# Performance work log

Hardware: AMD Instinct MI355X
Metric: run time of the kernel (lower is better)

The kernel has to match this reference:

```python
import jax, jax.numpy as jnp
import numpy as np

KEY_DIM = 64
SCALE_PER_SEQ = 1.0 / np.sqrt(KEY_DIM).astype(np.float32)
SCALE_OVER_SEQS = 1.0 / np.sqrt(KEY_DIM).astype(np.float32)


def setup_inputs() -> dict:
    key = jax.random.key(0)
    ks = jax.random.split(key, 6)
    b, i, t, j, d, dv, kd = 4, 512, 32, 256, 512, 512, KEY_DIM
    w_scale = 0.05
    return {
        "input_seq": jax.random.normal(ks[0], (b, i, d), jnp.float32),
        "memory_x": jax.random.normal(ks[1], (b, t, j, d), jnp.float32),
        "memory_y": jax.random.normal(ks[2], (b, t, j, dv), jnp.float32),
        "Wq": jax.random.normal(ks[3], (d, kd), jnp.float32) * w_scale,
        "bq": jnp.zeros((kd,), jnp.float32),
        "Wk": jax.random.normal(ks[4], (d, kd), jnp.float32) * w_scale,
        "bk": jnp.zeros((kd,), jnp.float32),
        "Wv": jax.random.normal(ks[5], (dv, dv), jnp.float32) * w_scale,
        "bv": jnp.zeros((dv,), jnp.float32),
    }


def reference(input_seq, memory_x, memory_y, Wq, bq, Wk, bk, Wv, bv):
    # Projections (Dense layers)
    queries = input_seq @ Wq + bq          # [b, i, kd]
    keys = memory_x @ Wk + bk              # [b, t, j, kd]
    values = memory_y @ Wv + bv            # [b, t, j, dv]

    # Level 1: within-sequence attention
    attn_mat = jnp.einsum('bik,btjk->btij', queries, keys)          # [b, t, i, j]
    per_seq_attn = jax.nn.softmax(SCALE_PER_SEQ * attn_mat, axis=-1)
    per_seq_retrieved = jnp.einsum('btij,btjk->btik', per_seq_attn, values)  # [b, t, i, dv]

    # Level 2: over-sequences attention (max-reduce over j, softmax over t)
    mem_seq_attn = jnp.max(attn_mat, axis=-1)                       # [b, t, i]
    mem_seq_attn = jax.nn.softmax(SCALE_OVER_SEQS * mem_seq_attn, axis=1)

    retrieved = jnp.einsum('bti,btik->bik', mem_seq_attn, per_seq_retrieved)  # [b, i, dv]
    return retrieved
```

## Files before the change

### kernel.cpp

```cpp
#include <hip/hip_runtime.h>
#include <cstdint>

#define B_ 4
#define I_ 512
#define T_ 32
#define J_ 256
#define D_ 512
#define DV_ 512
#define KD_ 64
#define TJ_ (T_*J_)
#define BI_ (B_*I_)
#define MK_ (B_*T_*J_)

typedef unsigned short u16;
typedef __attribute__((ext_vector_type(8))) u16 u16x8;
typedef __attribute__((ext_vector_type(4))) u16 u16x4;
typedef __attribute__((ext_vector_type(8))) short bf16x8;
typedef __attribute__((ext_vector_type(4))) float f32x4;

__device__ __forceinline__ u16 f2bf(float f){
  unsigned u = __float_as_uint(f);
  u += 0x7fffu + ((u >> 16) & 1u);
  return (u16)(u >> 16);
}
__device__ __forceinline__ float bf2f(u16 h){ return __uint_as_float(((unsigned)h) << 16); }

#define GLD16(gsrc, ldst) __builtin_amdgcn_global_load_lds( \
    (const __attribute__((address_space(1))) unsigned int*)(gsrc), \
    (__attribute__((address_space(3))) unsigned int*)(ldst), 16, 0, 0)

__global__ __launch_bounds__(256) void k_prep(const float* __restrict__ Y, u16* __restrict__ Yt,
                                              const float* __restrict__ Wq, const float* __restrict__ Wk,
                                              const float* __restrict__ Wv, u16* __restrict__ wqt,
                                              u16* __restrict__ wkt, u16* __restrict__ wvt){
  __shared__ __align__(16) u16 tileT[64][72];
  int bid = blockIdx.x;
  int tid = threadIdx.x;
  if (bid < 4096){
    int kx = bid & 127, ny = (bid >> 7) & 7, b = bid >> 10;
    int k0 = kx*64, n0 = ny*64;
    #pragma unroll
    for (int s=0;s<4;++s){
      int idx = tid + s*256; int r = idx>>4, c4 = idx&15;
      const float4 v = *(const float4*)&Y[((size_t)b*TJ_ + k0 + r)*DV_ + n0 + c4*4];
      tileT[c4*4+0][r] = f2bf(v.x);
      tileT[c4*4+1][r] = f2bf(v.y);
      tileT[c4*4+2][r] = f2bf(v.z);
      tileT[c4*4+3][r] = f2bf(v.w);
    }
    __syncthreads();
    #pragma unroll
    for (int s=0;s<2;++s){
      int idx = tid + s*256; int rn = idx>>3, c8 = idx&7;
      *(u16x8*)&Yt[((size_t)b*DV_ + n0 + rn)*TJ_ + k0 + c8*8] = *(const u16x8*)&tileT[rn][c8*8];
    }
  } else {
    int gid = (bid - 4096)*256 + tid;
    if (gid < 32768){
      int n = gid >> 9, k = gid & 511;
      wqt[gid] = f2bf(Wq[(size_t)k*64 + n]);
    } else if (gid < 65536){
      int g = gid - 32768;
      int n = g >> 9, k = g & 511;
      wkt[g] = f2bf(Wk[(size_t)k*64 + n]);
    } else {
      int g = gid - 65536;
      int n = g >> 9, k = g & 511;
      wvt[g] = f2bf(Wv[(size_t)k*512 + n]);
    }
  }
}

__global__ __launch_bounds__(256) void k_proj(const float* __restrict__ mx, const float* __restrict__ iseq,
                                              const u16* __restrict__ wkt, const u16* __restrict__ wqt,
                                              const float* __restrict__ bk, const float* __restrict__ bq,
                                              u16* __restrict__ kbf, u16* __restrict__ qbf){
  __shared__ __align__(16) u16 As[32][72];
  __shared__ __align__(16) u16 Bs[64][72];
  int bid = blockIdx.x;
  const float* A; const u16* Bt; const float* bias; u16* C; int row0;
  if (bid < 1024){ A = mx;   Bt = wkt; bias = bk; C = kbf; row0 = bid*32; }
  else           { A = iseq; Bt = wqt; bias = bq; C = qbf; row0 = (bid-1024)*32; }
  int tid = threadIdx.x;
  int lane = tid & 63, wv = tid >> 6;
  int lrow = lane & 15, lk8 = (lane >> 4) * 8;
  int mf = wv >> 1, nfb = (wv & 1) * 2;
  int ar = tid >> 4, ac4 = tid & 15;
  int br = tid >> 3, bc8 = tid & 7;
  f32x4 acc[2];
  acc[0] = (f32x4){0.f,0.f,0.f,0.f}; acc[1] = (f32x4){0.f,0.f,0.f,0.f};

  float4 fa[2][2]; u16x8 fb[2][2];
  #define PROJ_LOAD(pp, k0) { \
    fa[pp][0] = *(const float4*)&A[(size_t)(row0 + ar)*512 + (k0) + ac4*4]; \
    fa[pp][1] = *(const float4*)&A[(size_t)(row0 + ar + 16)*512 + (k0) + ac4*4]; \
    fb[pp][0] = *(const u16x8*)&Bt[(size_t)br*512 + (k0) + bc8*8]; \
    fb[pp][1] = *(const u16x8*)&Bt[(size_t)(br+32)*512 + (k0) + bc8*8]; }

  PROJ_LOAD(0, 0)
  #pragma unroll
  for (int t=0;t<8;++t){
    const int p = t & 1;
    if (t) __syncthreads();
    if (t < 7) PROJ_LOAD(p^1, (t+1)*64)
    #pragma unroll
    for (int s=0;s<2;++s){
      u16x4 o; o[0]=f2bf(fa[p][s].x); o[1]=f2bf(fa[p][s].y); o[2]=f2bf(fa[p][s].z); o[3]=f2bf(fa[p][s].w);
      *(u16x4*)&As[ar + 16*s][ac4*4] = o;
      *(u16x8*)&Bs[br + 32*s][bc8*8] = fb[p][s];
    }
    __syncthreads();
    #pragma unroll
    for (int kk=0;kk<2;++kk){
      bf16x8 a = *(const bf16x8*)&As[mf*16 + lrow][kk*32 + lk8];
      #pragma unroll
      for (int n2=0;n2<2;++n2){
        bf16x8 bb = *(const bf16x8*)&Bs[(nfb+n2)*16 + lrow][kk*32 + lk8];
        acc[n2] = __builtin_amdgcn_mfma_f32_16x16x32_bf16(a, bb, acc[n2], 0, 0, 0);
      }
    }
  }
  #undef PROJ_LOAD
  #pragma unroll
  for (int n2=0;n2<2;++n2)
    #pragma unroll
    for (int r=0;r<4;++r){
      int row = row0 + mf*16 + (lane>>4)*4 + r;
      int col = (nfb+n2)*16 + lrow;
      C[(size_t)row*64 + col] = f2bf(acc[n2][r] + bias[col]);
    }
}

__global__ __launch_bounds__(256) void k_score(const u16* __restrict__ Qbf, const u16* __restrict__ Kbf,
                                               u16* __restrict__ P, float* __restrict__ mb, float* __restrict__ zb){
  __shared__ __align__(16) u16 Qs[64][72];
  __shared__ __align__(16) u16 Ks[256][72];
  __shared__ float smax[4][64];
  __shared__ float ssum[4][64];
  __shared__ float mrow[64];
  int tid = threadIdx.x;
  int i0 = blockIdx.x*64, t = blockIdx.y, b = blockIdx.z;
  int lane = tid & 63, wv = tid >> 6;
  int lrow = lane & 15, lk = (lane >> 4) * 8;

  #pragma unroll
  for (int s=0;s<2;++s){
    int idx = tid + s*256; int r = idx>>3, c8 = idx&7;
    *(u16x8*)&Qs[r][c8*8] = *(const u16x8*)&Qbf[((size_t)b*I_ + i0 + r)*KD_ + c8*8];
  }
  #pragma unroll
  for (int s=0;s<8;++s){
    int idx = tid + s*256; int r = idx>>3, c8 = idx&7;
    *(u16x8*)&Ks[r][c8*8] = *(const u16x8*)&Kbf[(((size_t)b*T_ + t)*J_ + r)*KD_ + c8*8];
  }
  __syncthreads();

  f32x4 acc[4][4];
  #pragma unroll
  for (int i=0;i<4;++i)
    #pragma unroll
    for (int j=0;j<4;++j) acc[i][j] = (f32x4){0.f,0.f,0.f,0.f};

  #pragma unroll
  for (int kk=0;kk<2;++kk){
    bf16x8 a[4], bb[4];
    #pragma unroll
    for (int mf=0;mf<4;++mf) a[mf] = *(const bf16x8*)&Qs[mf*16 + lrow][kk*32 + lk];
    #pragma unroll
    for (int nf=0;nf<4;++nf) bb[nf] = *(const bf16x8*)&Ks[wv*64 + nf*16 + lrow][kk*32 + lk];
    #pragma unroll
    for (int mf=0;mf<4;++mf)
      #pragma unroll
      for (int nf=0;nf<4;++nf)
        acc[mf][nf] = __builtin_amdgcn_mfma_f32_16x16x32_bf16(a[mf], bb[nf], acc[mf][nf], 0, 0, 0);
  }

  #pragma unroll
  for (int mf=0;mf<4;++mf)
    #pragma unroll
    for (int r=0;r<4;++r){
      float v = acc[mf][0][r];
      #pragma unroll
      for (int nf=1;nf<4;++nf) v = fmaxf(v, acc[mf][nf][r]);
      v = fmaxf(v, __shfl_xor(v, 1));
      v = fmaxf(v, __shfl_xor(v, 2));
      v = fmaxf(v, __shfl_xor(v, 4));
      v = fmaxf(v, __shfl_xor(v, 8));
      if (lrow == 0) smax[wv][mf*16 + (lane>>4)*4 + r] = v;
    }
  __syncthreads();
  if (tid < 64){
    float m = fmaxf(fmaxf(smax[0][tid], smax[1][tid]), fmaxf(smax[2][tid], smax[3][tid]));
    mrow[tid] = m;
    mb[((size_t)b*T_ + t)*I_ + i0 + tid] = m;
  }
  __syncthreads();

  #pragma unroll
  for (int mf=0;mf<4;++mf)
    #pragma unroll
    for (int r=0;r<4;++r){
      int row = mf*16 + (lane>>4)*4 + r;
      float M = mrow[row];
      float ssm = 0.f;
      #pragma unroll
      for (int nf=0;nf<4;++nf){
        float p = __expf(0.125f*(acc[mf][nf][r] - M));
        acc[mf][nf][r] = p;
        ssm += p;
      }
      ssm += __shfl_xor(ssm, 1);
      ssm += __shfl_xor(ssm, 2);
      ssm += __shfl_xor(ssm, 4);
      ssm += __shfl_xor(ssm, 8);
      if (lrow == 0) ssum[wv][row] = ssm;
    }
  __syncthreads();
  if (tid < 64){
    float z = ssum[0][tid] + ssum[1][tid] + ssum[2][tid] + ssum[3][tid];
    zb[((size_t)b*T_ + t)*I_ + i0 + tid] = z;
  }

  u16* Ps = &Ks[0][0];
  #pragma unroll
  for (int mf=0;mf<4;++mf)
    #pragma unroll
    for (int nf=0;nf<4;++nf)
      #pragma unroll
      for (int r=0;r<4;++r){
        int row = mf*16 + (lane>>4)*4 + r;
        int col = wv*64 + nf*16 + lrow;
        Ps[row*264 + col] = f2bf(acc[mf][nf][r]);
      }
  __syncthreads();
  #pragma unroll
  for (int s=0;s<8;++s){
    int idx = tid + s*256; int r = idx>>5, c8 = idx&31;
    *(u16x8*)&P[(((size_t)b*T_ + t)*I_ + i0 + r)*J_ + c8*8] = *(const u16x8*)&Ps[r*264 + c8*8];
  }
}

template<int CH>
__global__ __launch_bounds__(256,2) void k_passB(const u16* __restrict__ P, const float* __restrict__ mbp,
                                                 const float* __restrict__ zbp, const u16* __restrict__ Yt,
                                                 u16* __restrict__ Up){
  constexpr int TPC = T_/CH;
  __shared__ __align__(16) u16 As[128*64];
  __shared__ __align__(16) u16 Bs[128*64];
  __shared__ float cs[TPC][128];
  int tid = threadIdx.x;
  int lane = tid & 63, wv = tid >> 6, wm = wv >> 1, wn = wv & 1;
  int lrow = lane & 15;

  int NWG = 16*B_*CH;
  int per = NWG >> 3;
  int logical = (blockIdx.x & 7)*per + (blockIdx.x >> 3);
  int group = logical >> 4, within = logical & 15;
  int ix = within & 3, ny = within >> 2;
  int b = group / CH, ch = group % CH;
  int i0 = ix*128, n0 = ny*128;

  if (tid < 128){
    int i = i0 + tid;
    float w[T_];
    float lmax = -3.0e38f;
    #pragma unroll
    for (int t=0;t<T_;++t){
      float mt = 0.125f * mbp[((size_t)b*T_ + t)*I_ + i];
      w[t] = mt;
      lmax = fmaxf(lmax, mt);
    }
    float W = 0.f;
    #pragma unroll
    for (int t=0;t<T_;++t){ float e = __expf(w[t] - lmax); w[t] = e; W += e; }
    float inv = 1.f / W;
    #pragma unroll
    for (int tt=0;tt<TPC;++tt)
      cs[tt][tid] = w[ch*TPC+tt] * inv / zbp[((size_t)b*T_ + ch*TPC + tt)*I_ + i];
  }
  __syncthreads();

  int l8 = lane >> 3, sl = lane & 7;

  f32x4 acc[4][4];
  #pragma unroll
  for (int i=0;i<4;++i)
    #pragma unroll
    for (int j=0;j<4;++j) acc[i][j] = (f32x4){0.f,0.f,0.f,0.f};

  for (int tt = 0; tt < TPC; ++tt){
    int t = ch*TPC + tt;
    const u16* Pbase = &P[(((size_t)b*T_ + t)*I_ + i0)*J_];
    const u16* Ybase = &Yt[((size_t)b*DV_ + n0)*TJ_ + (size_t)t*J_];
    f32x4 at[4][4];
    #pragma unroll
    for (int i=0;i<4;++i)
      #pragma unroll
      for (int j=0;j<4;++j) at[i][j] = (f32x4){0.f,0.f,0.f,0.f};

    for (int st = 0; st < 4; ++st){
      int j0 = st*64;
      if (tt | st) __syncthreads();
      #pragma unroll
      for (int s=0;s<4;++s){
        int row = (wv*4+s)*8 + l8;
        int colA = j0 + ((sl ^ (row & 7)) << 3);
        GLD16(Pbase + (size_t)row*J_ + colA, (u16*)As + (wv*4+s)*512);
        GLD16(Ybase + (size_t)row*TJ_ + colA, (u16*)Bs + (wv*4+s)*512);
      }
      __syncthreads();
      #pragma unroll
      for (int kk=0;kk<2;++kk){
        bf16x8 a[4], bb[4];
        #pragma unroll
        for (int mf=0;mf<4;++mf){
          int ar = wm*64 + mf*16 + lrow;
          int off = ar*128 + ((kk*64 + (lane>>4)*16) ^ ((ar & 7) << 4));
          a[mf] = *(const bf16x8*)((const char*)As + off);
        }
        #pragma unroll
        for (int nf=0;nf<4;++nf){
          int br = wn*64 + nf*16 + lrow;
          int off = br*128 + ((kk*64 + (lane>>4)*16) ^ ((br & 7) << 4));
          bb[nf] = *(const bf16x8*)((const char*)Bs + off);
        }
        #pragma unroll
        for (int mf=0;mf<4;++mf)
          #pragma unroll
          for (int nf=0;nf<4;++nf)
            at[mf][nf] = __builtin_amdgcn_mfma_f32_16x16x32_bf16(a[mf], bb[nf], at[mf][nf], 0, 0, 0);
      }
    }
    #pragma unroll
    for (int mf=0;mf<4;++mf)
      #pragma unroll
      for (int r=0;r<4;++r){
        float c = cs[tt][wm*64 + mf*16 + (lane>>4)*4 + r];
        #pragma unroll
        for (int nf=0;nf<4;++nf)
          acc[mf][nf][r] += c * at[mf][nf][r];
      }
  }

  #pragma unroll
  for (int mf=0;mf<4;++mf)
    #pragma unroll
    for (int nf=0;nf<4;++nf)
      #pragma unroll
      for (int r=0;r<4;++r){
        int row = i0 + wm*64 + mf*16 + (lane>>4)*4 + r;
        int col = n0 + wn*64 + nf*16 + lrow;
        Up[(size_t)ch*BI_*DV_ + ((size_t)b*I_ + row)*DV_ + col] = f2bf(acc[mf][nf][r]);
      }
}

template<int CH>
__global__ __launch_bounds__(256) void k_final(const u16* __restrict__ Up, const u16* __restrict__ Bt,
                                               const float* __restrict__ bv, float* __restrict__ out){
  __shared__ __align__(16) u16 As[32][72];
  __shared__ __align__(16) u16 Bs[64][72];
  int tid = threadIdx.x;
  int lane = tid & 63, wv = tid >> 6;
  int lrow = lane & 15, lk8 = (lane >> 4) * 8;
  int bid = blockIdx.x;
  int swz = (bid & 7)*64 + (bid >> 3);
  int row0 = (swz >> 3)*32, col0 = (swz & 7)*64;
  int mf = wv >> 1, nfb = (wv & 1)*2;
  const size_t S = (size_t)BI_*DV_;
  int ar = tid >> 3, ac8 = tid & 7;
  f32x4 acc[2];
  acc[0] = (f32x4){0.f,0.f,0.f,0.f}; acc[1] = (f32x4){0.f,0.f,0.f,0.f};

  u16x8 pa[2][CH]; u16x8 rb[2][2];
  #define FIN_LOAD(pp, k0) { \
    _Pragma("unroll") \
    for (int c=0;c<CH;++c) pa[pp][c] = *(const u16x8*)&Up[(size_t)c*S + (size_t)(row0+ar)*512 + (k0) + ac8*8]; \
    _Pragma("unroll") \
    for (int s=0;s<2;++s) rb[pp][s] = *(const u16x8*)&Bt[(size_t)(col0 + (tid>>3) + 32*s)*512 + (k0) + ac8*8]; }

  FIN_LOAD(0, 0)
  #pragma unroll
  for (int t=0;t<8;++t){
    const int p = t & 1;
    if (t) __syncthreads();
    if (t < 7) FIN_LOAD(p^1, (t+1)*64)
    u16x8 o;
    #pragma unroll
    for (int e=0;e<8;++e){
      float v = 0.f;
      #pragma unroll
      for (int c=0;c<CH;++c) v += bf2f(pa[p][c][e]);
      o[e] = f2bf(v);
    }
    *(u16x8*)&As[ar][ac8*8] = o;
    #pragma unroll
    for (int s=0;s<2;++s) *(u16x8*)&Bs[(tid>>3) + 32*s][ac8*8] = rb[p][s];
    __syncthreads();
    #pragma unroll
    for (int kk=0;kk<2;++kk){
      bf16x8 a = *(const bf16x8*)&As[mf*16 + lrow][kk*32 + lk8];
      #pragma unroll
      for (int n2=0;n2<2;++n2){
        bf16x8 bb = *(const bf16x8*)&Bs[(nfb+n2)*16 + lrow][kk*32 + lk8];
        acc[n2] = __builtin_amdgcn_mfma_f32_16x16x32_bf16(a, bb, acc[n2], 0, 0, 0);
      }
    }
  }
  #undef FIN_LOAD
  #pragma unroll
  for (int n2=0;n2<2;++n2)
    #pragma unroll
    for (int r=0;r<4;++r){
      int row = row0 + mf*16 + (lane>>4)*4 + r;
      int col = col0 + (nfb+n2)*16 + lrow;
      out[(size_t)row*DV_ + col] = acc[n2][r] + bv[col];
    }
}

extern "C" void kernel_launch(void* const* d_in, const int* in_sizes, int n_in,
                              void* d_out, int out_size, void* d_ws, size_t ws_size,
                              hipStream_t stream){
  const float* input_seq = (const float*)d_in[0];
  const float* memory_x  = (const float*)d_in[1];
  const float* memory_y  = (const float*)d_in[2];
  const float* Wq = (const float*)d_in[3];
  const float* bq = (const float*)d_in[4];
  const float* Wk = (const float*)d_in[5];
  const float* bk = (const float*)d_in[6];
  const float* Wv = (const float*)d_in[7];
  const float* bv = (const float*)d_in[8];
  float* out = (float*)d_out;

  char* ws = (char*)d_ws;
  size_t off = 0;
  auto alloc = [&](size_t bytes)->void*{
    void* p = ws + off; off += (bytes + 255) & ~(size_t)255; return p;
  };
  u16*   wqt = (u16*)  alloc((size_t)KD_*D_*2);
  u16*   wkt = (u16*)  alloc((size_t)KD_*D_*2);
  u16*   wvt = (u16*)  alloc((size_t)DV_*DV_*2);
  u16*   qbf = (u16*)  alloc((size_t)BI_*KD_*2);
  u16*   kbf = (u16*)  alloc((size_t)MK_*KD_*2);
  u16*   yt  = (u16*)  alloc((size_t)B_*DV_*TJ_*2);
  u16*   Pb  = (u16*)  alloc((size_t)B_*T_*I_*J_*2);
  float* mb  = (float*)alloc((size_t)B_*T_*I_*4);
  float* zb  = (float*)alloc((size_t)B_*T_*I_*4);
  u16*   Up  = (u16*)  alloc((size_t)8*BI_*DV_*2);

  k_prep<<<4096 + 1280, 256, 0, stream>>>(memory_y, yt, Wq, Wk, Wv, wqt, wkt, wvt);
  k_proj<<<1024 + 64, 256, 0, stream>>>(memory_x, input_seq, wkt, wqt, bk, bq, kbf, qbf);
  k_score<<<dim3(I_/64, T_, B_), 256, 0, stream>>>(qbf, kbf, Pb, mb, zb);
  k_passB<8><<<16*B_*8, 256, 0, stream>>>(Pb, mb, zb, yt, Up);
  k_final<8><<<512, 256, 0, stream>>>(Up, wvt, bv, out);
}
```

Before: 92.85 us.

## Double-buffer Y tiles, read P directly from global, rescale accumulators across t

The passB kernel now double-buffers the Y (values) tile in LDS, issuing the next step's loads before computing the current one. The P operand is read straight from global memory into registers instead of being staged through LDS. The per-t temporary accumulator is dropped: running accumulators are rescaled by the ratio of consecutive softmax coefficients and multiplied by the last coefficient at the end, which saves registers. Both the projection epilogue and the passB epilogue now stage output through LDS to get coalesced 16-byte stores. The ratio trick can lose precision or divide by zero if a coefficient underflows, and unstaged global P reads may be poorly coalesced.

After: 112.4 us. 21.1% more time.

```diff
diff --git a/kernel.cpp b/kernel.cpp
--- a/kernel.cpp
+++ b/kernel.cpp
@@ -121,14 +121,21 @@
     }
   }
   #undef PROJ_LOAD
+  __syncthreads();
+  u16* R = &As[0][0];
   #pragma unroll
   for (int n2=0;n2<2;++n2)
     #pragma unroll
     for (int r=0;r<4;++r){
-      int row = row0 + mf*16 + (lane>>4)*4 + r;
+      int row = mf*16 + (lane>>4)*4 + r;
       int col = (nfb+n2)*16 + lrow;
-      C[(size_t)row*64 + col] = f2bf(acc[n2][r] + bias[col]);
-    }
+      R[row*64 + col] = f2bf(acc[n2][r] + bias[col]);
+    }
+  __syncthreads();
+  {
+    int row = tid >> 3, c8 = tid & 7;
+    *(u16x8*)&C[(size_t)(row0+row)*64 + c8*8] = *(const u16x8*)&R[row*64 + c8*8];
+  }
 }
 
 __global__ __launch_bounds__(256) void k_score(const u16* __restrict__ Qbf, const u16* __restrict__ Kbf,
@@ -245,12 +252,12 @@
                                                  const float* __restrict__ zbp, const u16* __restrict__ Yt,
                                                  u16* __restrict__ Up){
   constexpr int TPC = T_/CH;
-  __shared__ __align__(16) u16 As[128*64];
-  __shared__ __align__(16) u16 Bs[128*64];
+  constexpr int NS = TPC*4;
+  __shared__ __align__(16) u16 Bsh[2][8192];
   __shared__ float cs[TPC][128];
   int tid = threadIdx.x;
   int lane = tid & 63, wv = tid >> 6, wm = wv >> 1, wn = wv & 1;
-  int lrow = lane & 15;
+  int lrow = lane & 15, lg = lane >> 4;
 
   int NWG = 16*B_*CH;
   int per = NWG >> 3;
@@ -260,6 +267,22 @@
   int b = group / CH, ch = group % CH;
   int i0 = ix*128, n0 = ny*128;
 
+  int l8 = lane >> 3, sl = lane & 7;
+
+  auto STAGEB = [&](int step, int pp){
+    int tt = step >> 2, st = step & 3;
+    int t = ch*TPC + tt, j0 = st*64;
+    const u16* Ybase = &Yt[((size_t)b*DV_ + n0)*TJ_ + (size_t)t*J_];
+    #pragma unroll
+    for (int s=0;s<4;++s){
+      int row = (wv*4+s)*8 + l8;
+      int colA = j0 + ((sl ^ (row & 7)) << 3);
+      GLD16(Ybase + (size_t)row*TJ_ + colA, (u16*)Bsh[pp] + (wv*4+s)*512);
+    }
+  };
+
+  STAGEB(0, 0);
+
   if (tid < 128){
     int i = i0 + tid;
     float w[T_];
@@ -280,8 +303,6 @@
   }
   __syncthreads();
 
-  int l8 = lane >> 3, sl = lane & 7;
-
   f32x4 acc[4][4];
   #pragma unroll
   for (int i=0;i<4;++i)
@@ -289,69 +310,68 @@
     for (int j=0;j<4;++j) acc[i][j] = (f32x4){0.f,0.f,0.f,0.f};
 
   for (int tt = 0; tt < TPC; ++tt){
+    if (tt){
+      #pragma unroll
+      for (int mf=0;mf<4;++mf)
+        #pragma unroll
+        for (int r=0;r<4;++r){
+          int row = wm*64 + mf*16 + lg*4 + r;
+          float ratio = cs[tt-1][row] / cs[tt][row];
+          #pragma unroll
+          for (int nf=0;nf<4;++nf) acc[mf][nf][r] *= ratio;
+        }
+    }
     int t = ch*TPC + tt;
     const u16* Pbase = &P[(((size_t)b*T_ + t)*I_ + i0)*J_];
-    const u16* Ybase = &Yt[((size_t)b*DV_ + n0)*TJ_ + (size_t)t*J_];
-    f32x4 at[4][4];
-    #pragma unroll
-    for (int i=0;i<4;++i)
-      #pragma unroll
-      for (int j=0;j<4;++j) at[i][j] = (f32x4){0.f,0.f,0.f,0.f};
-
+    #pragma unroll
     for (int st = 0; st < 4; ++st){
-      int j0 = st*64;
-      if (tt | st) __syncthreads();
-      #pragma unroll
-      for (int s=0;s<4;++s){
-        int row = (wv*4+s)*8 + l8;
-        int colA = j0 + ((sl ^ (row & 7)) << 3);
-        GLD16(Pbase + (size_t)row*J_ + colA, (u16*)As + (wv*4+s)*512);
-        GLD16(Ybase + (size_t)row*TJ_ + colA, (u16*)Bs + (wv*4+s)*512);
-      }
-      __syncthreads();
+      const int step = tt*4 + st;
+      const int pp = step & 1;
+      if (step + 1 < NS) STAGEB(step+1, pp^1);
+      const u16* Pj = Pbase + st*64;
       #pragma unroll
       for (int kk=0;kk<2;++kk){
         bf16x8 a[4], bb[4];
         #pragma unroll
-        for (int mf=0;mf<4;++mf){
-          int ar = wm*64 + mf*16 + lrow;
-          int off = ar*128 + ((kk*64 + (lane>>4)*16) ^ ((ar & 7) << 4));
-          a[mf] = *(const bf16x8*)((const char*)As + off);
-        }
+        for (int mf=0;mf<4;++mf)
+          a[mf] = *(const bf16x8*)&Pj[(size_t)(wm*64 + mf*16 + lrow)*J_ + kk*32 + lg*8];
         #pragma unroll
         for (int nf=0;nf<4;++nf){
           int br = wn*64 + nf*16 + lrow;
-          int off = br*128 + ((kk*64 + (lane>>4)*16) ^ ((br & 7) << 4));
-          bb[nf] = *(const bf16x8*)((const char*)Bs + off);
+          int off = br*128 + ((kk*64 + lg*16) ^ ((br & 7) << 4));
+          bb[nf] = *(const bf16x8*)((const char*)Bsh[pp] + off);
         }
         #pragma unroll
         for (int mf=0;mf<4;++mf)
           #pragma unroll
           for (int nf=0;nf<4;++nf)
-            at[mf][nf] = __builtin_amdgcn_mfma_f32_16x16x32_bf16(a[mf], bb[nf], at[mf][nf], 0, 0, 0);
-      }
-    }
-    #pragma unroll
-    for (int mf=0;mf<4;++mf)
-      #pragma unroll
-      for (int r=0;r<4;++r){
-        float c = cs[tt][wm*64 + mf*16 + (lane>>4)*4 + r];
-        #pragma unroll
-        for (int nf=0;nf<4;++nf)
-          acc[mf][nf][r] += c * at[mf][nf][r];
-      }
-  }
-
+            acc[mf][nf] = __builtin_amdgcn_mfma_f32_16x16x32_bf16(a[mf], bb[nf], acc[mf][nf], 0, 0, 0);
+      }
+      __syncthreads();
+    }
+  }
+
+  u16* R = (u16*)&Bsh[0][0];
   #pragma unroll
   for (int mf=0;mf<4;++mf)
     #pragma unroll
-    for (int nf=0;nf<4;++nf)
-      #pragma unroll
-      for (int r=0;r<4;++r){
-        int row = i0 + wm*64 + mf*16 + (lane>>4)*4 + r;
-        int col = n0 + wn*64 + nf*16 + lrow;
-        Up[(size_t)ch*BI_*DV_ + ((size_t)b*I_ + row)*DV_ + col] = f2bf(acc[mf][nf][r]);
-      }
+    for (int r=0;r<4;++r){
+      int row = wm*64 + mf*16 + lg*4 + r;
+      float cfin = cs[TPC-1][row];
+      #pragma unroll
+      for (int nf=0;nf<4;++nf){
+        int col = wn*64 + nf*16 + lrow;
+        R[row*128 + col] = f2bf(acc[mf][nf][r] * cfin);
+      }
+    }
+  __syncthreads();
+  u16* Ub = &Up[(size_t)ch*BI_*DV_ + ((size_t)b*I_ + i0)*DV_ + n0];
+  #pragma unroll
+  for (int s=0;s<8;++s){
+    int id = tid + s*256;
+    int row = id >> 4, c8 = id & 15;
+    *(u16x8*)&Ub[(size_t)row*DV_ + c8*8] = *(const u16x8*)&R[row*128 + c8*8];
+  }
 }
 
 template<int CH>
```
